# Optimization experiments

Hardware: AMD Instinct MI355X
Metric: run time of the kernel (lower is better)

## Reference

```python
import jax, jax.numpy as jnp
import numpy as np

B, T, N = 512, 1024, 64


def setup_inputs() -> dict:
    key = jax.random.key(0)
    k1, k2, k3 = jax.random.split(key, 3)
    unary = jax.random.normal(k1, (B, T, N), dtype=jnp.float32)
    lengths = jax.random.randint(k2, (B,), 1, T + 1)
    transitions = jax.random.normal(k3, (N, N), dtype=jnp.float32) * 0.1
    return {"unary": unary, "lengths": lengths, "transitions": transitions}


def reference(unary, lengths, transitions):
    # CRF log-partition (forward algorithm), same math as tf.contrib.crf.crf_log_norm.
    # unary: [B, T, N], lengths: [B], transitions: [N, N] -> logZ: [B]
    Bs, Ts, Ns = unary.shape
    lengths = jnp.maximum(lengths, 1)
    alpha0 = unary[:, 0, :]  # [B, N]

    # scan over time steps 1..T-1; freeze alpha once t >= length (dynamic_rnn semantics)
    unary_rest = jnp.swapaxes(unary[:, 1:, :], 0, 1)  # [T-1, B, N]
    ts = jnp.arange(1, Ts)

    def step(alpha, inp):
        u_t, t = inp
        # scores[b, i, j] = alpha[b, i] + transitions[i, j] + u_t[b, j]
        scores = alpha[:, :, None] + transitions[None, :, :] + u_t[:, None, :]
        new_alpha = jax.nn.logsumexp(scores, axis=1)  # [B, N]
        alpha = jnp.where((t < lengths)[:, None], new_alpha, alpha)
        return alpha, None

    alpha, _ = jax.lax.scan(step, alpha0, (unary_rest, ts))
    return jax.nn.logsumexp(alpha, axis=1)  # [B]
```

## Files before the change

### kernel.cpp

```cpp
#include <hip/hip_runtime.h>


typedef float f4 __attribute__((ext_vector_type(4)));

constexpr int Tt = 1024;
constexpr int Nn = 64;
constexpr int ES = 68;
constexpr float LOG2E = 1.44269504088896340736f;
constexpr float LN2   = 0.69314718055994530942f;

__global__ __launch_bounds__(128, 1) void crf_fwd(
    const float* __restrict__ unary,
    const int*   __restrict__ lengths,
    const float* __restrict__ trans,
    float*       __restrict__ out)
{
    const int b    = blockIdx.x;
    const int tid  = threadIdx.x;
    const int w    = tid >> 6;
    const int lane = tid & 63;

    __shared__ float Ecol[Nn * ES];
    __shared__ float Erow[Nn * ES];
    __shared__ f4    shp4[2][Nn / 4];
    __shared__ float shb[Nn];

    #pragma unroll
    for (int c = 0; c < (Nn * Nn) / 128; ++c) {
        int idx = c * 128 + tid;
        int i = idx >> 6, j = idx & 63;
        float e = __expf(trans[idx]);
        Erow[i * ES + j] = e;
        Ecol[j * ES + i] = e;
    }
    __syncthreads();

    const f4* eb = (const f4*)((w == 0) ? &Ecol[lane * ES] : &Erow[lane * ES]);
    f4 E0  = eb[0],  E1  = eb[1],  E2  = eb[2],  E3  = eb[3];
    f4 E4  = eb[4],  E5  = eb[5],  E6  = eb[6],  E7  = eb[7];
    f4 E8  = eb[8],  E9  = eb[9],  E10 = eb[10], E11 = eb[11];
    f4 E12 = eb[12], E13 = eb[13], E14 = eb[14], E15 = eb[15];

    int L = lengths[b];
    L = L < 1 ? 1 : (L > Tt ? Tt : L);
    const int m = (L - 1) >> 1;

    const float* ub = unary + (size_t)b * Tt * Nn;

    const int trips = (w == 0) ? m : (L - 1 - m);
    const int tbase = (w == 0) ? 1 : (L - 1);
    const int dir   = (w == 0) ? 1 : -1;

    float acc = (w == 0) ? ub[lane] * LOG2E : 0.0f;
    float* myp = (float*)shp4[w];
    const f4* pp = shp4[w];

    float u_cur[4];
    {
        int smax = trips > 0 ? trips - 1 : 0;
        #pragma unroll
        for (int k = 0; k < 4; ++k) {
            int sc = k < smax ? k : smax;
            u_cur[k] = ub[(tbase + dir * sc) * Nn + lane] * LOG2E;
        }
    }

    for (int s0 = 0; s0 < trips; s0 += 4) {
        float u_nxt[4];
        #pragma unroll
        for (int k = 0; k < 4; ++k) {
            int sc = s0 + 4 + k;
            if (sc > trips - 1) sc = trips - 1;
            u_nxt[k] = ub[(tbase + dir * sc) * Nn + lane] * LOG2E;
        }

        #pragma unroll
        for (int k = 0; k < 4; ++k) {
            if (s0 + k >= trips) break;

            float ui = (w != 0) ? u_cur[k] : 0.0f;
            float uo = (w == 0) ? u_cur[k] : 0.0f;

            float tmpv = acc + ui;
            float sf = __uint_as_float(
                (unsigned)__builtin_amdgcn_readfirstlane((int)__float_as_uint(tmpv)));
            float p = __builtin_amdgcn_exp2f(tmpv - sf);

            myp[lane] = p;

            f4 q0  = pp[0],  q1  = pp[1],  q2  = pp[2],  q3  = pp[3];
            f4 q4  = pp[4],  q5  = pp[5],  q6  = pp[6],  q7  = pp[7];
            f4 q8  = pp[8],  q9  = pp[9],  q10 = pp[10], q11 = pp[11];
            f4 q12 = pp[12], q13 = pp[13], q14 = pp[14], q15 = pp[15];
            asm volatile("" : "+v"(q0),  "+v"(q1),  "+v"(q2),  "+v"(q3),
                              "+v"(q4),  "+v"(q5),  "+v"(q6),  "+v"(q7),
                              "+v"(q8),  "+v"(q9),  "+v"(q10), "+v"(q11),
                              "+v"(q12), "+v"(q13), "+v"(q14), "+v"(q15));

            f4 A0 = {0.f, 0.f, 0.f, 0.f};
            f4 A1 = {0.f, 0.f, 0.f, 0.f};
            f4 A2 = {0.f, 0.f, 0.f, 0.f};
            f4 A3 = {0.f, 0.f, 0.f, 0.f};
            A0 = q0  * E0  + A0;  A1 = q1  * E1  + A1;
            A2 = q2  * E2  + A2;  A3 = q3  * E3  + A3;
            A0 = q4  * E4  + A0;  A1 = q5  * E5  + A1;
            A2 = q6  * E6  + A2;  A3 = q7  * E7  + A3;
            A0 = q8  * E8  + A0;  A1 = q9  * E9  + A1;
            A2 = q10 * E10 + A2;  A3 = q11 * E11 + A3;
            A0 = q12 * E12 + A0;  A1 = q13 * E13 + A1;
            A2 = q14 * E14 + A2;  A3 = q15 * E15 + A3;
            f4 S = (A0 + A1) + (A2 + A3);
            float z = (S.x + S.y) + (S.z + S.w);

            acc = sf + uo + __builtin_amdgcn_logf(z);
        }

        #pragma unroll
        for (int k = 0; k < 4; ++k) u_cur[k] = u_nxt[k];
    }

    if (w == 1) shb[lane] = acc;
    __syncthreads();
    if (w == 0) {
        float v = acc + shb[lane];
        float mx = v;
        #pragma unroll
        for (int k = 32; k >= 1; k >>= 1)
            mx = fmaxf(mx, __shfl_xor(mx, k, 64));
        float ssum = __builtin_amdgcn_exp2f(v - mx);
        #pragma unroll
        for (int k = 32; k >= 1; k >>= 1)
            ssum += __shfl_xor(ssum, k, 64);
        if (lane == 0) out[b] = LN2 * (mx + __builtin_amdgcn_logf(ssum));
    }
}

extern "C" void kernel_launch(void* const* d_in, const int* in_sizes, int n_in,
                              void* d_out, int out_size, void* d_ws, size_t ws_size,
                              hipStream_t stream) {
    const float* unary   = (const float*)d_in[0];
    const int*   lengths = (const int*)d_in[1];
    const float* trans   = (const float*)d_in[2];
    float*       out     = (float*)d_out;

    const int Bb = in_sizes[1];
    crf_fwd<<<Bb, 128, 0, stream>>>(unary, lengths, trans, out);
}
```

Before: 309.4 us.

## Run CRF forward recursion in linear domain with periodic exponent renormalization

Keeps alpha in the probability (linear) domain instead of log domain. Each step then costs a multiply and the matvec, with no per-step exp2/log/readfirstlane on the critical serial path. Every 4 steps the value is rescaled by a power of two taken from lane 0's exponent, and the exponent is tracked in an integer offset. This shortens the per-step dependency chain, but it risks underflow or overflow within the 4-step window if values across lanes span a large dynamic range.

Result: faster. 296.9 us (-4.1%).

```diff
diff --git a/kernel.cpp b/kernel.cpp
--- a/kernel.cpp
+++ b/kernel.cpp
@@ -6,8 +6,7 @@
 constexpr int Tt = 1024;
 constexpr int Nn = 64;
 constexpr int ES = 68;
-constexpr float LOG2E = 1.44269504088896340736f;
-constexpr float LN2   = 0.69314718055994530942f;
+constexpr float LN2 = 0.69314718055994530942f;
 
 __global__ __launch_bounds__(128, 1) void crf_fwd(
     const float* __restrict__ unary,
@@ -24,6 +23,7 @@
     __shared__ float Erow[Nn * ES];
     __shared__ f4    shp4[2][Nn / 4];
     __shared__ float shb[Nn];
+    __shared__ int   sh_off_b;
 
     #pragma unroll
     for (int c = 0; c < (Nn * Nn) / 128; ++c) {
@@ -51,42 +51,38 @@
     const int tbase = (w == 0) ? 1 : (L - 1);
     const int dir   = (w == 0) ? 1 : -1;
 
-    float acc = (w == 0) ? ub[lane] * LOG2E : 0.0f;
+    float acc = (w == 0) ? __expf(ub[lane]) : 1.0f;
+    int   off = 0;
     float* myp = (float*)shp4[w];
     const f4* pp = shp4[w];
 
-    float u_cur[4];
+    float w_cur[4];
     {
         int smax = trips > 0 ? trips - 1 : 0;
         #pragma unroll
         for (int k = 0; k < 4; ++k) {
             int sc = k < smax ? k : smax;
-            u_cur[k] = ub[(tbase + dir * sc) * Nn + lane] * LOG2E;
+            w_cur[k] = __expf(ub[(tbase + dir * sc) * Nn + lane]);
         }
     }
 
     for (int s0 = 0; s0 < trips; s0 += 4) {
-        float u_nxt[4];
+        float w_nxt[4];
         #pragma unroll
         for (int k = 0; k < 4; ++k) {
             int sc = s0 + 4 + k;
             if (sc > trips - 1) sc = trips - 1;
-            u_nxt[k] = ub[(tbase + dir * sc) * Nn + lane] * LOG2E;
+            w_nxt[k] = __expf(ub[(tbase + dir * sc) * Nn + lane]);
         }
 
         #pragma unroll
         for (int k = 0; k < 4; ++k) {
             if (s0 + k >= trips) break;
 
-            float ui = (w != 0) ? u_cur[k] : 0.0f;
-            float uo = (w == 0) ? u_cur[k] : 0.0f;
+            float win  = (w != 0) ? w_cur[k] : 1.0f;
+            float wout = (w == 0) ? w_cur[k] : 1.0f;
 
-            float tmpv = acc + ui;
-            float sf = __uint_as_float(
-                (unsigned)__builtin_amdgcn_readfirstlane((int)__float_as_uint(tmpv)));
-            float p = __builtin_amdgcn_exp2f(tmpv - sf);
-
-            myp[lane] = p;
+            myp[lane] = acc * win;
 
             f4 q0  = pp[0],  q1  = pp[1],  q2  = pp[2],  q3  = pp[3];
             f4 q4  = pp[4],  q5  = pp[5],  q6  = pp[6],  q7  = pp[7];
@@ -112,26 +108,36 @@
             f4 S = (A0 + A1) + (A2 + A3);
             float z = (S.x + S.y) + (S.z + S.w);
 
-            acc = sf + uo + __builtin_amdgcn_logf(z);
+            acc = z * wout;
+        }
+
+        {
+            unsigned s0b = (unsigned)__builtin_amdgcn_readfirstlane(
+                (int)__float_as_uint(acc));
+            int e = (int)((s0b >> 23) & 0xFF) - 127;
+            off += e;
+            acc *= __uint_as_float((unsigned)(127 - e) << 23);
         }
 
         #pragma unroll
-        for (int k = 0; k < 4; ++k) u_cur[k] = u_nxt[k];
+        for (int k = 0; k < 4; ++k) w_cur[k] = w_nxt[k];
     }
 
-    if (w == 1) shb[lane] = acc;
+    if (w == 1) {
+        shb[lane] = acc;
+        if (lane == 0) sh_off_b = off;
+    }
     __syncthreads();
     if (w == 0) {
-        float v = acc + shb[lane];
-        float mx = v;
-        #pragma unroll
-        for (int k = 32; k >= 1; k >>= 1)
-            mx = fmaxf(mx, __shfl_xor(mx, k, 64));
-        float ssum = __builtin_amdgcn_exp2f(v - mx);
+        float v = acc * shb[lane];
+        float ssum = v;
         #pragma unroll
         for (int k = 32; k >= 1; k >>= 1)
             ssum += __shfl_xor(ssum, k, 64);
-        if (lane == 0) out[b] = LN2 * (mx + __builtin_amdgcn_logf(ssum));
+        if (lane == 0) {
+            float l2 = __builtin_amdgcn_logf(ssum);
+            out[b] = LN2 * ((float)(off + sh_off_b) + l2);
+        }
     }
 }
 
```
